# Optimization experiments

Hardware: AMD Instinct MI355X
Metric: run time of the kernel (lower is better)

Reference implementation:

```python
import jax, jax.numpy as jnp
import numpy as np

SEQ, B, H, NP, HN = 2048, 2, 2048, 16, 128
SCALE = 1.0 / 11.313708498984761  # 1/sqrt(128), hardcoded in the source baddbmm


def setup_inputs() -> dict:
    key = jax.random.key(0)
    k1, k2, k3 = jax.random.split(key, 3)
    return {
        "hidden_states": jax.random.normal(k1, (SEQ, B, H), dtype=jnp.float32),
        "w_qkv": jax.random.normal(k2, (3 * H, H), dtype=jnp.float32) * 0.02,
        "w_out": jax.random.normal(k3, (H, H), dtype=jnp.float32) * 0.02,
    }


def reference(hidden_states, w_qkv, w_out):
    s, b, h = hidden_states.shape
    # QKV projection (column-parallel linear, no bias): [s, b, 3h]
    qkv = hidden_states @ w_qkv.T
    # [s, b, np, 3*hn] then split (num_query_groups == num_heads)
    qkv = qkv.reshape(s, b, NP, 3 * HN)
    q, k, v = qkv[..., :HN], qkv[..., HN:2 * HN], qkv[..., 2 * HN:]
    # baddbmm QK^T with alpha = 1/sqrt(128): scores [b, np, sq, sk]
    scores = jnp.einsum("sbnh,tbnh->bnst", q, k) * SCALE
    # scale_t == 1 then plain softmax (fallback path; no mask applied)
    prob = jax.nn.softmax(scores, axis=-1)
    # context: bmm(prob, V) -> [sq, b, np, hn] -> [sq, b, h]
    ctx = jnp.einsum("bnst,tbnh->sbnh", prob, v).reshape(s, b, h)
    # row-parallel output linear (no bias)
    return ctx @ w_out.T
```

## Files before the change

kernel.cpp:

```cpp
#include <hip/hip_runtime.h>
#include <stdint.h>

#define SEQ 2048
#define BATCH 2
#define HID 2048
#define NHEADS 16
#define HDIM 128
#define QKV_LD 6144
#define SCALE_F 0.08838834764831845f
#define LOG2E_F 1.4426950408889634f

typedef unsigned short u16;
using bf16x8 = __attribute__((ext_vector_type(8))) short;
using f32x4  = __attribute__((ext_vector_type(4))) float;

__device__ inline u16 f2bf(float f) {
  union { float f; uint32_t u; } c; c.f = f;
  uint32_t u = c.u;
  uint32_t r = (u + 0x7fffu + ((u >> 16) & 1u)) >> 16;
  return (u16)r;
}

__device__ inline void gl_lds16(const u16* g, u16* l) {
  __builtin_amdgcn_global_load_lds((const __attribute__((address_space(1))) void*)g,
                                   (__attribute__((address_space(3))) void*)l,
                                   16, 0, 0);
}

__global__ void cvt_all(const float* __restrict__ hs, const float* __restrict__ wqkv,
                        const float* __restrict__ wout, u16* __restrict__ ws_out) {
  int i = blockIdx.x * blockDim.x + threadIdx.x;
  const float* src;
  int j;
  float sc = 1.0f;
  if (i < 2097152) { src = hs; j = i; }
  else if (i < 5242880) {
    j = i - 2097152; src = wqkv;
    const int f = j >> 9;
    if ((f % 384) < 128) sc = SCALE_F;
  } else { j = i - 5242880; src = wout; }
  float4 v = ((const float4*)src)[j];
  ushort4 o;
  o.x = f2bf(v.x * sc); o.y = f2bf(v.y * sc); o.z = f2bf(v.z * sc); o.w = f2bf(v.w * sc);
  ((ushort4*)ws_out)[i] = o;
}

#define QK_M 4096
#define QK_N 6144
#define QK_K 2048
#define QK_T (QK_K / 64)

__global__ __launch_bounds__(512, 2)
void gemm256_qkv(const u16* __restrict__ A, const u16* __restrict__ Bw,
                 u16* __restrict__ Cout, u16* __restrict__ vt) {
  __shared__ __align__(16) u16 As[2][16384];
  __shared__ __align__(16) u16 Bs[2][16384];
  const int bm = blockIdx.x, bn = blockIdx.y;
  const int tid = threadIdx.x;
  const int wave = tid >> 6, lane = tid & 63;
  const int quad = lane >> 4, l16 = lane & 15;
  const int wm = (wave >> 2) * 128, wn = (wave & 3) * 64;
  f32x4 acc[8][4] = {};

  const u16* Ablk = A + (size_t)(bm * 256) * QK_K;
  const u16* Bblk = Bw + (size_t)(bn * 256) * QK_K;

  auto stageA = [&](int t, int ks, int buf) {
    #pragma unroll
    for (int p = 0; p < 2; ++p) {
      int j = p * 512 + tid;
      int row = ((j >> 6) << 4) + (j & 15);
      int c = (j >> 4) & 3;
      gl_lds16(Ablk + (size_t)row * QK_K + t * 64 + ks * 32 + c * 8,
               &As[buf][ks * 8192 + (p * 512 + wave * 64) * 8]);
    }
  };
  auto stageB = [&](int t, int ks, int buf) {
    #pragma unroll
    for (int p = 0; p < 2; ++p) {
      int j = p * 512 + tid;
      int row = ((j >> 6) << 4) + (j & 15);
      int c = (j >> 4) & 3;
      gl_lds16(Bblk + (size_t)row * QK_K + t * 64 + ks * 32 + c * 8,
               &Bs[buf][ks * 8192 + (p * 512 + wave * 64) * 8]);
    }
  };

  stageA(0, 0, 0); stageB(0, 0, 0);
  stageA(0, 1, 0); stageB(0, 1, 0);
  stageA(1, 0, 1); stageB(1, 0, 1);
  asm volatile("s_waitcnt vmcnt(8)" ::: "memory");
  __builtin_amdgcn_s_barrier();
  __builtin_amdgcn_sched_barrier(0);

  for (int t = 0; t < QK_T; ++t) {
    const int cb = t & 1;
    const u16* Ab = &As[cb][0];
    const u16* Bb = &Bs[cb][0];
    bf16x8 af[4], bfr[4];

    #pragma unroll
    for (int mt = 0; mt < 4; ++mt) {
      int row = wm + mt * 16 + l16;
      af[mt] = *(const bf16x8*)&Ab[(((row >> 4) << 6) + quad * 16 + (row & 15)) * 8];
    }
    #pragma unroll
    for (int nt = 0; nt < 4; ++nt) {
      int row = wn + nt * 16 + l16;
      bfr[nt] = *(const bf16x8*)&Bb[(((row >> 4) << 6) + quad * 16 + (row & 15)) * 8];
    }
    if (t + 1 < QK_T) stageA(t + 1, 1, cb ^ 1);
    __builtin_amdgcn_s_barrier();
    __builtin_amdgcn_s_setprio(1);
    #pragma unroll
    for (int mt = 0; mt < 4; ++mt)
      #pragma unroll
      for (int nt = 0; nt < 4; ++nt)
        acc[mt][nt] = __builtin_amdgcn_mfma_f32_16x16x32_bf16(af[mt], bfr[nt], acc[mt][nt], 0, 0, 0);
    __builtin_amdgcn_s_setprio(0);
    __builtin_amdgcn_s_barrier();

    #pragma unroll
    for (int mt = 0; mt < 4; ++mt) {
      int row = wm + 64 + mt * 16 + l16;
      af[mt] = *(const bf16x8*)&Ab[(((row >> 4) << 6) + quad * 16 + (row & 15)) * 8];
    }
    if (t + 1 < QK_T) stageB(t + 1, 1, cb ^ 1);
    __builtin_amdgcn_s_barrier();
    __builtin_amdgcn_s_setprio(1);
    #pragma unroll
    for (int mt = 0; mt < 4; ++mt)
      #pragma unroll
      for (int nt = 0; nt < 4; ++nt)
        acc[4 + mt][nt] = __builtin_amdgcn_mfma_f32_16x16x32_bf16(af[mt], bfr[nt], acc[4 + mt][nt], 0, 0, 0);
    __builtin_amdgcn_s_setprio(0);
    if (t < QK_T - 1) asm volatile("s_waitcnt vmcnt(8)" ::: "memory");
    else              asm volatile("s_waitcnt vmcnt(0)" ::: "memory");
    __builtin_amdgcn_s_barrier();
    __builtin_amdgcn_sched_barrier(0);

    #pragma unroll
    for (int mt = 0; mt < 4; ++mt) {
      int row = wm + mt * 16 + l16;
      af[mt] = *(const bf16x8*)&Ab[8192 + (((row >> 4) << 6) + quad * 16 + (row & 15)) * 8];
    }
    #pragma unroll
    for (int nt = 0; nt < 4; ++nt) {
      int row = wn + nt * 16 + l16;
      bfr[nt] = *(const bf16x8*)&Bb[8192 + (((row >> 4) << 6) + quad * 16 + (row & 15)) * 8];
    }
    if (t + 2 < QK_T) stageA(t + 2, 0, cb);
    __builtin_amdgcn_s_barrier();
    __builtin_amdgcn_s_setprio(1);
    #pragma unroll
    for (int mt = 0; mt < 4; ++mt)
      #pragma unroll
      for (int nt = 0; nt < 4; ++nt)
        acc[mt][nt] = __builtin_amdgcn_mfma_f32_16x16x32_bf16(af[mt], bfr[nt], acc[mt][nt], 0, 0, 0);
    __builtin_amdgcn_s_setprio(0);
    __builtin_amdgcn_s_barrier();

    #pragma unroll
    for (int mt = 0; mt < 4; ++mt) {
      int row = wm + 64 + mt * 16 + l16;
      af[mt] = *(const bf16x8*)&Ab[8192 + (((row >> 4) << 6) + quad * 16 + (row & 15)) * 8];
    }
    if (t + 2 < QK_T) stageB(t + 2, 0, cb);
    __builtin_amdgcn_s_barrier();
    __builtin_amdgcn_s_setprio(1);
    #pragma unroll
    for (int mt = 0; mt < 4; ++mt)
      #pragma unroll
      for (int nt = 0; nt < 4; ++nt)
        acc[4 + mt][nt] = __builtin_amdgcn_mfma_f32_16x16x32_bf16(af[mt], bfr[nt], acc[4 + mt][nt], 0, 0, 0);
    __builtin_amdgcn_s_setprio(0);
    if (t < QK_T - 2)       asm volatile("s_waitcnt vmcnt(8)" ::: "memory");
    else if (t == QK_T - 2) asm volatile("s_waitcnt vmcnt(4)" ::: "memory");
    else                    asm volatile("s_waitcnt vmcnt(0)" ::: "memory");
    __builtin_amdgcn_s_barrier();
    __builtin_amdgcn_sched_barrier(0);
  }

  #pragma unroll
  for (int ntf = 0; ntf < 4; ++ntf) {
    const int coff = wn + ntf * 16;
    const int g = bn * 2 + (coff >> 7);
    const int h = g / 3;
    if ((g % 3) == 2) {
      const int hd = (coff & 127) + l16;
      u16* vt0 = vt + ((size_t)h * HDIM) * SEQ;
      u16* vt1 = vt + ((size_t)(NHEADS + h) * HDIM) * SEQ;
      #pragma unroll
      for (int mt = 0; mt < 8; ++mt) {
        const int s0 = (bm * 256 + wm + mt * 16 + quad * 4) >> 1;
        uint32_t w0 = (uint32_t)f2bf(acc[mt][ntf][0]) | ((uint32_t)f2bf(acc[mt][ntf][2]) << 16);
        uint32_t w1 = (uint32_t)f2bf(acc[mt][ntf][1]) | ((uint32_t)f2bf(acc[mt][ntf][3]) << 16);
        *(uint32_t*)&vt0[(size_t)hd * SEQ + s0] = w0;
        *(uint32_t*)&vt1[(size_t)hd * SEQ + s0] = w1;
      }
    } else {
      const int col = bn * 256 + coff + l16;
      #pragma unroll
      for (int mt = 0; mt < 8; ++mt)
        #pragma unroll
        for (int r = 0; r < 4; ++r) {
          const int row = bm * 256 + wm + mt * 16 + quad * 4 + r;
          Cout[(size_t)row * QK_N + col] = f2bf(acc[mt][ntf][r]);
        }
    }
  }
}

template<int MODE>
__global__ __launch_bounds__(256)
void gemm_bt(const u16* __restrict__ A, const u16* __restrict__ Bw,
             void* __restrict__ Cout, u16* __restrict__ vt, int M, int N, int K) {
  __shared__ __align__(16) u16 Asx[128 * 64];
  __shared__ __align__(16) u16 Bsx[128 * 64];
  const int bm = blockIdx.x, bn = blockIdx.y;
  const int tid = threadIdx.x;
  const int wave = tid >> 6, lane = tid & 63;
  const int quad = lane >> 4, l16 = lane & 15;
  const int wm = (wave >> 1) * 64, wn = (wave & 1) * 64;
  f32x4 acc[4][4] = {};

  const u16* Ablk = A + (size_t)(bm * 128) * K;
  const u16* Bblk = Bw + (size_t)(bn * 128) * K;

  for (int k0 = 0; k0 < K; k0 += 64) {
    __syncthreads();
    #pragma unroll
    for (int p = 0; p < 4; ++p) {
      int j = p * 256 + tid;
      int r = j >> 3, cs = j & 7, c = cs ^ (r & 7);
      gl_lds16(Ablk + (size_t)r * K + k0 + c * 8, Asx + (p * 256 + wave * 64) * 8);
      gl_lds16(Bblk + (size_t)r * K + k0 + c * 8, Bsx + (p * 256 + wave * 64) * 8);
    }
    __syncthreads();
    #pragma unroll
    for (int ks = 0; ks < 2; ++ks) {
      bf16x8 af[4], bfr[4];
      #pragma unroll
      for (int mt = 0; mt < 4; ++mt) {
        int row = wm + mt * 16 + l16;
        int cc = (ks * 4 + quad) ^ (row & 7);
        af[mt] = *(const bf16x8*)&Asx[(row * 8 + cc) * 8];
      }
      #pragma unroll
      for (int nt = 0; nt < 4; ++nt) {
        int row = wn + nt * 16 + l16;
        int cc = (ks * 4 + quad) ^ (row & 7);
        bfr[nt] = *(const bf16x8*)&Bsx[(row * 8 + cc) * 8];
      }
      #pragma unroll
      for (int mt = 0; mt < 4; ++mt)
        #pragma unroll
        for (int nt = 0; nt < 4; ++nt)
          acc[mt][nt] = __builtin_amdgcn_mfma_f32_16x16x32_bf16(af[mt], bfr[nt], acc[mt][nt], 0, 0, 0);
    }
  }

  #pragma unroll
  for (int mt = 0; mt < 4; ++mt)
    #pragma unroll
    for (int nt = 0; nt < 4; ++nt)
      #pragma unroll
      for (int r = 0; r < 4; ++r) {
        int row = bm * 128 + wm + mt * 16 + quad * 4 + r;
        int col = bn * 128 + wn + nt * 16 + l16;
        float v = acc[mt][nt][r];
        if (MODE == 1) ((u16*)Cout)[(size_t)row * N + col] = f2bf(v);
        else           ((float*)Cout)[(size_t)row * N + col] = v;
      }
}

__global__ __launch_bounds__(512, 2)
void attn(const u16* __restrict__ qkv, const u16* __restrict__ vt_g, u16* __restrict__ ctx) {
  const int qt = blockIdx.x, head = blockIdx.y, b = blockIdx.z;
  const int q0 = qt * 256;
  __shared__ __align__(16) u16 Ks[64 * 128];
  __shared__ __align__(16) u16 Vt[144 * 64];
  __shared__ __align__(16) u16 PsT[256 * 64];
  const int tid = threadIdx.x;
  const int wave = tid >> 6, lane = tid & 63;
  const int quad = lane >> 4, l16 = lane & 15;

  const u16* qkv_bh = qkv + (size_t)b * QKV_LD + head * 384;
  const u16* vt = vt_g + (size_t)(b * NHEADS + head) * HDIM * SEQ;

  if (tid < 128) {
    const int row = 128 + (tid >> 3), c = tid & 7;
    const u16 v = (row == 128) ? (u16)0x3F80 : (u16)0;
    ushort4 q4; q4.x = v; q4.y = v; q4.z = v; q4.w = v;
    *(ushort4*)&Vt[(row * 8 + c) * 8] = q4;
    *(ushort4*)&Vt[(row * 8 + c) * 8 + 4] = q4;
  }

  bf16x8 qf[2][4];
  #pragma unroll
  for (int h = 0; h < 4; ++h) {
    __syncthreads();
    #pragma unroll
    for (int p = 0; p < 2; ++p) {
      int j = p * 512 + tid;
      int r = j >> 4, cs = j & 15, c = cs ^ (r & 7);
      gl_lds16(qkv_bh + (size_t)(q0 + h * 64 + r) * (BATCH * QKV_LD) + c * 8,
               Ks + (p * 512 + wave * 64) * 8);
    }
    __syncthreads();
    if ((wave >> 1) == h) {
      #pragma unroll
      for (int nt = 0; nt < 2; ++nt)
        #pragma unroll
        for (int ks = 0; ks < 4; ++ks) {
          int row = (wave & 1) * 32 + nt * 16 + l16;
          int cc = (ks * 4 + quad) ^ (row & 7);
          qf[nt][ks] = *(const bf16x8*)&Ks[(row * 16 + cc) * 8];
        }
    }
  }

  f32x4 ot[9][2] = {};

  for (int kt = 0; kt < SEQ; kt += 64) {
    __syncthreads();
    #pragma unroll
    for (int p = 0; p < 2; ++p) {
      int j = p * 512 + tid;
      int r = j >> 4, cs = j & 15, c = cs ^ (r & 7);
      gl_lds16(qkv_bh + (size_t)(kt + r) * (BATCH * QKV_LD) + 128 + c * 8,
               Ks + (p * 512 + wave * 64) * 8);
    }
    #pragma unroll
    for (int p = 0; p < 2; ++p) {
      int j = p * 512 + tid;
      int hd = j >> 3, cs = j & 7, c = cs ^ (hd & 7);
      gl_lds16(vt + (size_t)hd * SEQ + kt + c * 8,
               Vt + (p * 512 + wave * 64) * 8);
    }
    __syncthreads();

    f32x4 st[4][2] = {};
    #pragma unroll
    for (int ks = 0; ks < 4; ++ks) {
      bf16x8 kf[4];
      #pragma unroll
      for (int mt = 0; mt < 4; ++mt) {
        int key = mt * 16 + l16;
        int cc = (ks * 4 + quad) ^ (key & 7);
        kf[mt] = *(const bf16x8*)&Ks[(key * 16 + cc) * 8];
      }
      #pragma unroll
      for (int mt = 0; mt < 4; ++mt)
        #pragma unroll
        for (int nt = 0; nt < 2; ++nt)
          st[mt][nt] = __builtin_amdgcn_mfma_f32_16x16x32_bf16(kf[mt], qf[nt][ks], st[mt][nt], 0, 0, 0);
    }

    #pragma unroll
    for (int mt = 0; mt < 4; ++mt)
      #pragma unroll
      for (int nt = 0; nt < 2; ++nt) {
        ushort4 pk;
        union { float f; uint32_t u; } cv;
        cv.f = __builtin_amdgcn_exp2f(st[mt][nt][0] * LOG2E_F); pk.x = (u16)(cv.u >> 16);
        cv.f = __builtin_amdgcn_exp2f(st[mt][nt][1] * LOG2E_F); pk.y = (u16)(cv.u >> 16);
        cv.f = __builtin_amdgcn_exp2f(st[mt][nt][2] * LOG2E_F); pk.z = (u16)(cv.u >> 16);
        cv.f = __builtin_amdgcn_exp2f(st[mt][nt][3] * LOG2E_F); pk.w = (u16)(cv.u >> 16);
        const int q = wave * 32 + nt * 16 + l16;
        const int kc = mt * 2 + (quad >> 1);
        *(ushort4*)&PsT[q * 64 + ((kc ^ (l16 & 7)) * 8 + (quad & 1) * 4)] = pk;
      }

    #pragma unroll
    for (int ks = 0; ks < 2; ++ks) {
      bf16x8 pf[2], vf[9];
      #pragma unroll
      for (int nt = 0; nt < 2; ++nt) {
        const int q = wave * 32 + nt * 16 + l16;
        const int cc = (ks * 4 + quad) ^ (l16 & 7);
        pf[nt] = *(const bf16x8*)&PsT[q * 64 + cc * 8];
      }
      #pragma unroll
      for (int mt = 0; mt < 9; ++mt) {
        const int hd = mt * 16 + l16;
        const int cc = (ks * 4 + quad) ^ (hd & 7);
        vf[mt] = *(const bf16x8*)&Vt[(hd * 8 + cc) * 8];
      }
      #pragma unroll
      for (int mt = 0; mt < 9; ++mt)
        #pragma unroll
        for (int nt = 0; nt < 2; ++nt)
          ot[mt][nt] = __builtin_amdgcn_mfma_f32_16x16x32_bf16(vf[mt], pf[nt], ot[mt][nt], 0, 0, 0);
    }
  }

  #pragma unroll
  for (int nt = 0; nt < 2; ++nt) {
    const float lv = __shfl(ot[8][nt][0], l16);
    const float inv_l = 1.0f / lv;
    const int s = q0 + wave * 32 + nt * 16 + l16;
    u16* dst = ctx + ((size_t)s * BATCH + b) * HID + head * HDIM;
    #pragma unroll
    for (int mt = 0; mt < 8; ++mt) {
      ushort4 w;
      w.x = f2bf(ot[mt][nt][0] * inv_l);
      w.y = f2bf(ot[mt][nt][1] * inv_l);
      w.z = f2bf(ot[mt][nt][2] * inv_l);
      w.w = f2bf(ot[mt][nt][3] * inv_l);
      *(ushort4*)&dst[mt * 16 + quad * 4] = w;
    }
  }
}

extern "C" void kernel_launch(void* const* d_in, const int* in_sizes, int n_in,
                              void* d_out, int out_size, void* d_ws, size_t ws_size,
                              hipStream_t stream) {
  const float* hs   = (const float*)d_in[0];
  const float* wqkv = (const float*)d_in[1];
  const float* wout = (const float*)d_in[2];
  float* out = (float*)d_out;
  char* ws = (char*)d_ws;

  u16* hs_bf   = (u16*)(ws);
  u16* wqkv_bf = (u16*)(ws + 16777216);
  u16* wout_bf = (u16*)(ws + 41943040);
  u16* qkv_bf  = (u16*)(ws + 50331648);
  u16* vt_bf   = (u16*)(ws + 100663296);
  u16* ctx_bf  = hs_bf;

  cvt_all<<<24576, 256, 0, stream>>>(hs, wqkv, wout, (u16*)ws);

  gemm256_qkv<<<dim3(16, 24), 512, 0, stream>>>(hs_bf, wqkv_bf, qkv_bf, vt_bf);

  attn<<<dim3(8, NHEADS, BATCH), 512, 0, stream>>>(qkv_bf, vt_bf, ctx_bf);

  gemm_bt<0><<<dim3(32, 16), 256, 0, stream>>>(ctx_bf, wout_bf, out, nullptr, 4096, 2048, 2048);
}
```

Baseline: 429.4 us.

## Double-buffer K/V tiles in attention and prefetch the next tile during compute

```diff
diff --git a/kernel.cpp b/kernel.cpp
--- a/kernel.cpp
+++ b/kernel.cpp
@@ -91,7 +91,6 @@
   stageA(1, 0, 1); stageB(1, 0, 1);
   asm volatile("s_waitcnt vmcnt(8)" ::: "memory");
   __builtin_amdgcn_s_barrier();
-  __builtin_amdgcn_sched_barrier(0);
 
   for (int t = 0; t < QK_T; ++t) {
     const int cb = t & 1;
@@ -137,7 +136,6 @@
     if (t < QK_T - 1) asm volatile("s_waitcnt vmcnt(8)" ::: "memory");
     else              asm volatile("s_waitcnt vmcnt(0)" ::: "memory");
     __builtin_amdgcn_s_barrier();
-    __builtin_amdgcn_sched_barrier(0);
 
     #pragma unroll
     for (int mt = 0; mt < 4; ++mt) {
@@ -178,7 +176,6 @@
     else if (t == QK_T - 2) asm volatile("s_waitcnt vmcnt(4)" ::: "memory");
     else                    asm volatile("s_waitcnt vmcnt(0)" ::: "memory");
     __builtin_amdgcn_s_barrier();
-    __builtin_amdgcn_sched_barrier(0);
   }
 
   #pragma unroll
@@ -211,10 +208,9 @@
   }
 }
 
-template<int MODE>
 __global__ __launch_bounds__(256)
-void gemm_bt(const u16* __restrict__ A, const u16* __restrict__ Bw,
-             void* __restrict__ Cout, u16* __restrict__ vt, int M, int N, int K) {
+void gemm_out(const u16* __restrict__ A, const u16* __restrict__ Bw,
+              float* __restrict__ Cout, int M, int N, int K) {
   __shared__ __align__(16) u16 Asx[128 * 64];
   __shared__ __align__(16) u16 Bsx[128 * 64];
   const int bm = blockIdx.x, bn = blockIdx.y;
@@ -268,9 +264,7 @@
       for (int r = 0; r < 4; ++r) {
         int row = bm * 128 + wm + mt * 16 + quad * 4 + r;
         int col = bn * 128 + wn + nt * 16 + l16;
-        float v = acc[mt][nt][r];
-        if (MODE == 1) ((u16*)Cout)[(size_t)row * N + col] = f2bf(v);
-        else           ((float*)Cout)[(size_t)row * N + col] = v;
+        Cout[(size_t)row * N + col] = acc[mt][nt][r];
       }
 }
 
@@ -278,8 +272,8 @@
 void attn(const u16* __restrict__ qkv, const u16* __restrict__ vt_g, u16* __restrict__ ctx) {
   const int qt = blockIdx.x, head = blockIdx.y, b = blockIdx.z;
   const int q0 = qt * 256;
-  __shared__ __align__(16) u16 Ks[64 * 128];
-  __shared__ __align__(16) u16 Vt[144 * 64];
+  __shared__ __align__(16) u16 Ks[2][64 * 128];
+  __shared__ __align__(16) u16 Vt[2][144 * 64];
   __shared__ __align__(16) u16 PsT[256 * 64];
   const int tid = threadIdx.x;
   const int wave = tid >> 6, lane = tid & 63;
@@ -292,8 +286,11 @@
     const int row = 128 + (tid >> 3), c = tid & 7;
     const u16 v = (row == 128) ? (u16)0x3F80 : (u16)0;
     ushort4 q4; q4.x = v; q4.y = v; q4.z = v; q4.w = v;
-    *(ushort4*)&Vt[(row * 8 + c) * 8] = q4;
-    *(ushort4*)&Vt[(row * 8 + c) * 8 + 4] = q4;
+    #pragma unroll
+    for (int bb = 0; bb < 2; ++bb) {
+      *(ushort4*)&Vt[bb][(row * 8 + c) * 8] = q4;
+      *(ushort4*)&Vt[bb][(row * 8 + c) * 8 + 4] = q4;
+    }
   }
 
   bf16x8 qf[2][4];
@@ -305,7 +302,7 @@
       int j = p * 512 + tid;
       int r = j >> 4, cs = j & 15, c = cs ^ (r & 7);
       gl_lds16(qkv_bh + (size_t)(q0 + h * 64 + r) * (BATCH * QKV_LD) + c * 8,
-               Ks + (p * 512 + wave * 64) * 8);
+               Ks[0] + (p * 512 + wave * 64) * 8);
     }
     __syncthreads();
     if ((wave >> 1) == h) {
@@ -315,30 +312,39 @@
         for (int ks = 0; ks < 4; ++ks) {
           int row = (wave & 1) * 32 + nt * 16 + l16;
           int cc = (ks * 4 + quad) ^ (row & 7);
-          qf[nt][ks] = *(const bf16x8*)&Ks[(row * 16 + cc) * 8];
+          qf[nt][ks] = *(const bf16x8*)&Ks[0][(row * 16 + cc) * 8];
         }
     }
   }
 
-  f32x4 ot[9][2] = {};
-
-  for (int kt = 0; kt < SEQ; kt += 64) {
-    __syncthreads();
+  auto stageKV = [&](int kt, int bb) {
     #pragma unroll
     for (int p = 0; p < 2; ++p) {
       int j = p * 512 + tid;
       int r = j >> 4, cs = j & 15, c = cs ^ (r & 7);
       gl_lds16(qkv_bh + (size_t)(kt + r) * (BATCH * QKV_LD) + 128 + c * 8,
-               Ks + (p * 512 + wave * 64) * 8);
+               Ks[bb] + (p * 512 + wave * 64) * 8);
     }
     #pragma unroll
     for (int p = 0; p < 2; ++p) {
       int j = p * 512 + tid;
       int hd = j >> 3, cs = j & 7, c = cs ^ (hd & 7);
       gl_lds16(vt + (size_t)hd * SEQ + kt + c * 8,
-               Vt + (p * 512 + wave * 64) * 8);
-    }
-    __syncthreads();
+               Vt[bb] + (p * 512 + wave * 64) * 8);
+    }
+  };
+
+  f32x4 ot[9][2] = {};
+
+  __syncthreads();
+  stageKV(0, 0);
+  __syncthreads();
+
+  for (int it = 0; it < SEQ / 64; ++it) {
+    const int cur = it & 1;
+    if (it + 1 < SEQ / 64) stageKV((it + 1) * 64, cur ^ 1);
+    const u16* Kb = Ks[cur];
+    const u16* Vb = Vt[cur];
 
     f32x4 st[4][2] = {};
     #pragma unroll
@@ -348,13 +354,15 @@
       for (int mt = 0; mt < 4; ++mt) {
         int key = mt * 16 + l16;
         int cc = (ks * 4 + quad) ^ (key & 7);
-        kf[mt] = *(const bf16x8*)&Ks[(key * 16 + cc) * 8];
-      }
+        kf[mt] = *(const bf16x8*)&Kb[(key * 16 + cc) * 8];
+      }
+      __builtin_amdgcn_s_setprio(1);
       #pragma unroll
       for (int mt = 0; mt < 4; ++mt)
         #pragma unroll
         for (int nt = 0; nt < 2; ++nt)
           st[mt][nt] = __builtin_amdgcn_mfma_f32_16x16x32_bf16(kf[mt], qf[nt][ks], st[mt][nt], 0, 0, 0);
+      __builtin_amdgcn_s_setprio(0);
     }
 
     #pragma unroll
@@ -385,14 +393,18 @@
       for (int mt = 0; mt < 9; ++mt) {
         const int hd = mt * 16 + l16;
         const int cc = (ks * 4 + quad) ^ (hd & 7);
-        vf[mt] = *(const bf16x8*)&Vt[(hd * 8 + cc) * 8];
-      }
+        vf[mt] = *(const bf16x8*)&Vb[(hd * 8 + cc) * 8];
+      }
+      __builtin_amdgcn_s_setprio(1);
       #pragma unroll
       for (int mt = 0; mt < 9; ++mt)
         #pragma unroll
         for (int nt = 0; nt < 2; ++nt)
           ot[mt][nt] = __builtin_amdgcn_mfma_f32_16x16x32_bf16(vf[mt], pf[nt], ot[mt][nt], 0, 0, 0);
-    }
+      __builtin_amdgcn_s_setprio(0);
+    }
+
+    __syncthreads();
   }
 
   #pragma unroll
@@ -435,5 +447,5 @@
 
   attn<<<dim3(8, NHEADS, BATCH), 512, 0, stream>>>(qkv_bf, vt_bf, ctx_bf);
 
-  gemm_bt<0><<<dim3(32, 16), 256, 0, stream>>>(ctx_bf, wout_bf, out, nullptr, 4096, 2048, 2048);
-}
+  gemm_out<<<dim3(32, 16), 256, 0, stream>>>(ctx_bf, wout_bf, out, 4096, 2048, 2048);
+}
```

New measurement: 419.0 us. 2.4% less time.
